# Performance work log

Measured on AMD Instinct MI355X. Metric: run time of the kernel, lower is better.

Reference implementation:

```python
import jax, jax.numpy as jnp
import numpy as np

D_MODEL = 512
N_HEADS = 8
D_HEAD = D_MODEL // N_HEADS  # 64
D_PROJ = 32
H_ENC = 512
D_MAX = 32


def _rope_cache(T, d):
    pos = jnp.arange(T, dtype=jnp.float32)[:, None]                      # [T,1]
    freqs = 1.0 / (10000.0 ** (jnp.arange(0, d, 2, dtype=jnp.float32) / d))  # [d/2]
    ang = pos * freqs                                                     # [T,d/2]
    return jnp.cos(ang), jnp.sin(ang)


def _apply_rope(x, cos, sin):
    # x: [B,H,T,D]
    T = x.shape[2]
    d2 = x.shape[-1] // 2
    x1, x2 = x[..., :d2], x[..., d2:]
    c = cos[:T][None, None]
    s = sin[:T][None, None]
    return jnp.concatenate([x1 * c - x2 * s, x2 * c + x1 * s], axis=-1)


def _layernorm(a, g, b, eps=1e-5):
    m = jnp.mean(a, axis=-1, keepdims=True)
    v = jnp.mean((a - m) ** 2, axis=-1, keepdims=True)
    return (a - m) * jax.lax.rsqrt(v + eps) * g + b


def setup_inputs() -> dict:
    key = jax.random.key(0)
    ks = jax.random.split(key, 8)
    B, T = 2, 2048
    x = jax.random.normal(ks[0], (B, T, D_MODEL), jnp.float32)
    q_projs = jax.random.normal(ks[1], (N_HEADS, D_MODEL, D_PROJ), jnp.float32) * D_MODEL ** -0.5
    k_projs = jax.random.normal(ks[2], (N_HEADS, D_MODEL, D_PROJ), jnp.float32) * D_MODEL ** -0.5
    w_v = jax.random.normal(ks[3], (D_MODEL, D_MODEL), jnp.float32) * D_MODEL ** -0.5
    w_proj = jax.random.normal(ks[4], (D_MODEL, D_MODEL), jnp.float32) * 0.02
    q_gain = jnp.ones((N_HEADS,), jnp.float32)
    enc_w0 = jax.random.normal(ks[5], (H_ENC, D_MODEL), jnp.float32) * D_MODEL ** -0.5
    enc_ln1_g = jnp.ones((H_ENC,), jnp.float32)
    enc_ln1_b = jnp.zeros((H_ENC,), jnp.float32)
    enc_w1 = jax.random.normal(ks[6], (H_ENC, H_ENC), jnp.float32) * H_ENC ** -0.5
    enc_ln2_g = jnp.ones((H_ENC,), jnp.float32)
    enc_ln2_b = jnp.zeros((H_ENC,), jnp.float32)
    enc_w2 = jax.random.normal(ks[7], (H_ENC, H_ENC), jnp.float32) * H_ENC ** -0.5
    enc_w_out = jax.random.normal(jax.random.fold_in(key, 99), (D_MAX, H_ENC), jnp.float32) * H_ENC ** -0.5
    coord_temp = jnp.ones((D_MAX,), jnp.float32)
    return {"x": x, "q_projs": q_projs, "k_projs": k_projs, "w_v": w_v, "w_proj": w_proj,
            "q_gain": q_gain, "enc_w0": enc_w0, "enc_ln1_g": enc_ln1_g, "enc_ln1_b": enc_ln1_b,
            "enc_w1": enc_w1, "enc_ln2_g": enc_ln2_g, "enc_ln2_b": enc_ln2_b, "enc_w2": enc_w2,
            "enc_w_out": enc_w_out, "coord_temp": coord_temp}


def reference(x, q_projs, k_projs, w_v, w_proj, q_gain,
              enc_w0, enc_ln1_g, enc_ln1_b, enc_w1, enc_ln2_g, enc_ln2_b,
              enc_w2, enc_w_out, coord_temp):
    B, T, C = x.shape
    # ---- CausalSelfAttention (qk_mode='per_head_proj') ----
    q = jnp.einsum('btd,hdo->bhto', x, q_projs)                    # [B,H,T,Dp]
    k = jnp.einsum('btd,hdo->bhto', x, k_projs)                    # [B,H,T,Dp]
    v = (x @ w_v.T).reshape(B, T, N_HEADS, D_HEAD).transpose(0, 2, 1, 3)  # [B,H,T,Dh]
    cos, sin = _rope_cache(T, D_PROJ)
    q = _apply_rope(q, cos, sin)
    k = _apply_rope(k, cos, sin)
    q = q * q_gain[None, :, None, None]
    scale = 1.0 / jnp.sqrt(jnp.asarray(D_PROJ, q.dtype))
    scores = jnp.einsum('bhto,bhso->bhts', q, k) * scale           # [B,H,T,T]
    causal = jnp.tril(jnp.ones((T, T), bool))
    scores = jnp.where(causal, scores, jnp.asarray(-1e30, scores.dtype))
    attn = jax.nn.softmax(scores, axis=-1)
    y = jnp.einsum('bhts,bhsd->bhtd', attn, v)                     # [B,H,T,Dh]
    # self-alignment subtraction (F.normalize eps = 1e-12)
    v_norm = v / jnp.maximum(jnp.linalg.norm(v, axis=-1, keepdims=True), 1e-12)
    self_align = jnp.sum(y * v_norm, axis=-1, keepdims=True) * v_norm
    y = y - self_align
    y = y.transpose(0, 2, 1, 3).reshape(B, T, C)
    h = x + y @ w_proj.T                                           # residual
    # ---- ChartEncoder (d_in == H so proj0 is Identity) ----
    he = h @ enc_w0.T
    he = h + jax.nn.silu(_layernorm(he, enc_ln1_g, enc_ln1_b) @ enc_w1.T)
    he = he + jax.nn.silu(_layernorm(he, enc_ln2_g, enc_ln2_b) @ enc_w2.T)
    h_rms = he * jax.lax.rsqrt(jnp.mean(he * he, axis=-1, keepdims=True) + 1e-6)
    z_raw = h_rms @ enc_w_out.T                                    # [B,T,d_max]
    z = jnp.tanh(z_raw / (jax.nn.softplus(coord_temp) + 1e-4))
    return z
```

## Files before the change

kernel.cpp:

```cpp
#include <hip/hip_runtime.h>
#include <math.h>

typedef unsigned short u16;
typedef __attribute__((ext_vector_type(8))) short short8;
typedef __attribute__((ext_vector_type(4))) float floatx4;

__device__ __forceinline__ float b2f(u16 u) { return __uint_as_float(((unsigned)u) << 16); }
__device__ __forceinline__ u16 f2b(float f) {
  unsigned u = __float_as_uint(f);
  return (u16)((u + 0x7fffu + ((u >> 16) & 1u)) >> 16);
}

__global__ __launch_bounds__(256) void prep_cast(const float* __restrict__ x, const float* __restrict__ wpr,
                                                 const float* __restrict__ w0, const float* __restrict__ w1,
                                                 const float* __restrict__ w2, const float* __restrict__ qp,
                                                 const float* __restrict__ kp, const float* __restrict__ wv,
                                                 u16* __restrict__ XB, u16* __restrict__ WPRb,
                                                 u16* __restrict__ W0b, u16* __restrict__ W1b,
                                                 u16* __restrict__ W2b, u16* __restrict__ wcat) {
  int bi = blockIdx.x, tid = threadIdx.x;
  if (bi < 2048) {
    int i = bi * 256 + tid;
    float4 v = ((const float4*)x)[i];
    ushort4 o; o.x = f2b(v.x); o.y = f2b(v.y); o.z = f2b(v.z); o.w = f2b(v.w);
    ((ushort4*)XB)[i] = o;
  } else if (bi < 3072) {
    int i = (bi - 2048) * 256 + tid;
    int sel = i >> 16, j = i & 65535;
    const float* s = sel == 0 ? wpr : sel == 1 ? w0 : sel == 2 ? w1 : w2;
    float4 v = ((const float4*)s)[j];
    ushort4 o; o.x = f2b(v.x); o.y = f2b(v.y); o.z = f2b(v.z); o.w = f2b(v.w);
    if (sel == 0) {
      ((ushort4*)WPRb)[j] = o;
    } else {
      u16* d = sel == 1 ? W0b : sel == 2 ? W1b : W2b;
      int n = j >> 7, k4 = (j & 127) << 2;
      int lane = (((k4 >> 3) & 3) << 4) | (n & 15);
      int dst = (((n >> 4) * 16 + (k4 >> 5)) << 9) + lane * 8 + (k4 & 7);
      *(ushort4*)(d + dst) = o;
    }
  } else {
    int i = (bi - 3072) * 256 + tid;
    int d = i & 511, c = i >> 9;
    float v;
    if (c < 512) {
      int hh = c >> 5, o = c & 31;
      const float* src = (hh < 8) ? qp : kp;
      int h = hh & 7;
      v = src[(h * 512 + d) * 32 + o];
    } else {
      v = wv[(c - 512) * 512 + d];
    }
    wcat[i] = f2b(v);
  }
}

template <int EPI, bool DUAL>
__global__ __launch_bounds__(256) void mgemm(const u16* __restrict__ A, const u16* __restrict__ Bw,
                                             const float* __restrict__ X, float* __restrict__ C,
                                             u16* __restrict__ Cb, int N) {
  __shared__ u16 As[64][72];
  __shared__ u16 Bs[64][72];
  const int tid = threadIdx.x;
  const int bm = blockIdx.y, bn = blockIdx.x;
  const int lane = tid & 63, wave = tid >> 6;
  const int wm = wave >> 1, wn = wave & 1;
  const int quad = lane >> 4, l16 = lane & 15;
  const int sr = tid >> 2;
  const int sk = (tid & 3) << 4;
  floatx4 acc[2][2] = {};
  const u16* Ap = A + (size_t)(bm * 64 + sr) * 512 + sk;
  const u16* Bp = Bw + (size_t)(bn * 64 + sr) * 512 + sk;
  uint4 a0 = *(const uint4*)(Ap);
  uint4 a1 = *(const uint4*)(Ap + 8);
  uint4 b0 = *(const uint4*)(Bp);
  uint4 b1 = *(const uint4*)(Bp + 8);
  for (int k0 = 0; k0 < 512; k0 += 64) {
    __syncthreads();
    *(uint4*)&As[sr][sk] = a0;
    *(uint4*)&As[sr][sk + 8] = a1;
    *(uint4*)&Bs[sr][sk] = b0;
    *(uint4*)&Bs[sr][sk + 8] = b1;
    __syncthreads();
    if (k0 + 64 < 512) {
      a0 = *(const uint4*)(Ap + k0 + 64);
      a1 = *(const uint4*)(Ap + k0 + 72);
      b0 = *(const uint4*)(Bp + k0 + 64);
      b1 = *(const uint4*)(Bp + k0 + 72);
    }
#pragma unroll
    for (int kk = 0; kk < 2; kk++) {
      short8 af0 = *(const short8*)&As[wm * 32 + l16][kk * 32 + quad * 8];
      short8 af1 = *(const short8*)&As[wm * 32 + 16 + l16][kk * 32 + quad * 8];
      short8 bf0 = *(const short8*)&Bs[wn * 32 + l16][kk * 32 + quad * 8];
      short8 bf1 = *(const short8*)&Bs[wn * 32 + 16 + l16][kk * 32 + quad * 8];
      acc[0][0] = __builtin_amdgcn_mfma_f32_16x16x32_bf16(af0, bf0, acc[0][0], 0, 0, 0);
      acc[0][1] = __builtin_amdgcn_mfma_f32_16x16x32_bf16(af0, bf1, acc[0][1], 0, 0, 0);
      acc[1][0] = __builtin_amdgcn_mfma_f32_16x16x32_bf16(af1, bf0, acc[1][0], 0, 0, 0);
      acc[1][1] = __builtin_amdgcn_mfma_f32_16x16x32_bf16(af1, bf1, acc[1][1], 0, 0, 0);
    }
  }
#pragma unroll
  for (int mt = 0; mt < 2; mt++)
#pragma unroll
    for (int r = 0; r < 4; r++) {
      int row = bm * 64 + wm * 32 + mt * 16 + quad * 4 + r;
#pragma unroll
      for (int nt = 0; nt < 2; nt++) {
        int col = bn * 64 + wn * 32 + nt * 16 + l16;
        float v = acc[mt][nt][r];
        if (EPI == 1) {
          v += X[(size_t)row * 512 + col];
        } else if (EPI == 2) {
          float xv = X[(size_t)row * 512 + col];
          v = xv + v / (1.f + __expf(-v));
        }
        C[(size_t)row * N + col] = v;
        if (DUAL) Cb[(size_t)row * N + col] = f2b(v);
      }
    }
}

__global__ __launch_bounds__(256) void prep_attn(const float* __restrict__ qkv, const float* __restrict__ qgain,
                                                 u16* __restrict__ qr, u16* __restrict__ kr,
                                                 u16* __restrict__ Vt) {
  const int bi = blockIdx.x, tid = threadIdx.x;
  if (bi < 2048) {
    int gid = bi * 256 + tid;
    int o = gid & 15;
    int t = (gid >> 4) & 2047;
    int h = (gid >> 15) & 7;
    int b = gid >> 18;
    const float* row = qkv + (size_t)(b * 2048 + t) * 1024;
    float freq = powf(10000.f, -(float)o / 16.f);
    float ang = (float)t * freq;
    float s, c;
    sincosf(ang, &s, &c);
    float g = qgain[h] * (0.17677669529663687f * 1.4426950408889634f);
    int qb = h * 32;
    float q0 = row[qb + o], q1 = row[qb + o + 16];
    float k0 = row[256 + qb + o], k1 = row[256 + qb + o + 16];
    u16* qo = qr + ((size_t)((b * 8 + h) * 2048 + t)) * 32;
    u16* ko = kr + ((size_t)((b * 8 + h) * 2048 + t)) * 32;
    qo[o] = f2b((q0 * c - q1 * s) * g);
    qo[o + 16] = f2b((q1 * c + q0 * s) * g);
    ko[o] = f2b(k0 * c - k1 * s);
    ko[o + 16] = f2b(k1 * c + k0 * s);
  } else {
    int idx = bi - 2048;
    const int tt = idx & 31, bh = idx >> 5;
    const int b = bh >> 3, h = bh & 7;
    __shared__ u16 Ts[64][72];
    const int r = tid >> 2, q = tid & 3;
    const float* src = qkv + ((size_t)(b * 2048 + tt * 64 + r)) * 1024 + 512 + h * 64 + q * 16;
#pragma unroll
    for (int j = 0; j < 4; j++) {
      float4 v = *(const float4*)(src + j * 4);
      Ts[q * 16 + j * 4 + 0][r] = f2b(v.x);
      Ts[q * 16 + j * 4 + 1][r] = f2b(v.y);
      Ts[q * 16 + j * 4 + 2][r] = f2b(v.z);
      Ts[q * 16 + j * 4 + 3][r] = f2b(v.w);
    }
    __syncthreads();
    u16* dst = Vt + ((size_t)(bh * 64 + r)) * 2048 + tt * 64 + q * 16;
    *(uint4*)dst = *(const uint4*)&Ts[r][q * 16];
    *(uint4*)(dst + 8) = *(const uint4*)&Ts[r][q * 16 + 8];
  }
}

__global__ __launch_bounds__(256) void attn_split(const u16* __restrict__ Qb, const u16* __restrict__ Kb,
                                                  const u16* __restrict__ Vt, float* __restrict__ PO,
                                                  float* __restrict__ PL) {
  const int bi = blockIdx.x;
  const int bh = bi & 15;
  const int q0i = (bi >> 4) & 15;
  const int rem = bi >> 8;
  const int qt = (rem & 1) ? (31 - q0i) : q0i;
  const int s = rem >> 1;
  const int tid = threadIdx.x;
  const int w = tid >> 6, lane = tid & 63, quad = lane >> 4, l16 = lane & 15;
  __shared__ u16 Vts[64][72];
  __shared__ u16 Ps[4][16][72];

  const int mid = (qt + 1) >> 1;
  const int kt_beg = s ? mid : 0;
  const int kt_end = s ? (qt + 1) : mid;

  short8 qfrag = *(const short8*)(Qb + ((size_t)(bh * 2048 + qt * 64 + w * 16 + l16)) * 32 + quad * 8);
  floatx4 o_acc[4] = {};
  float l_part[4] = {0.f, 0.f, 0.f, 0.f};
  const u16* Kbase = Kb + (size_t)bh * 2048 * 32;
  const u16* Vtb = Vt + (size_t)bh * 64 * 2048;
  const int vr = tid >> 2, vc = (tid & 3) << 4;

  uint4 v0 = {}, v1 = {};
  short8 kf[4] = {};
  if (kt_beg < kt_end) {
    const u16* src = Vtb + (size_t)vr * 2048 + kt_beg * 64 + vc;
    v0 = *(const uint4*)src;
    v1 = *(const uint4*)(src + 8);
#pragma unroll
    for (int nt = 0; nt < 4; nt++)
      kf[nt] = *(const short8*)(Kbase + (size_t)(kt_beg * 64 + nt * 16 + l16) * 32 + quad * 8);
  }

  for (int kt = kt_beg; kt < kt_end; ++kt) {
    __syncthreads();
    *(uint4*)&Vts[vr][vc] = v0;
    *(uint4*)&Vts[vr][vc + 8] = v1;
    __syncthreads();
    const bool more = (kt + 1 < kt_end);
    uint4 v0n = {}, v1n = {};
    short8 kfn[4] = {};
    if (more) {
      const u16* src = Vtb + (size_t)vr * 2048 + (kt + 1) * 64 + vc;
      v0n = *(const uint4*)src;
      v1n = *(const uint4*)(src + 8);
#pragma unroll
      for (int nt = 0; nt < 4; nt++)
        kfn[nt] = *(const short8*)(Kbase + (size_t)((kt + 1) * 64 + nt * 16 + l16) * 32 + quad * 8);
    }

    floatx4 s_acc[4];
#pragma unroll
    for (int nt = 0; nt < 4; nt++) {
      floatx4 zz = {0.f, 0.f, 0.f, 0.f};
      s_acc[nt] = __builtin_amdgcn_mfma_f32_16x16x32_bf16(qfrag, kf[nt], zz, 0, 0, 0);
    }
    const bool diag = (kt == qt);
#pragma unroll
    for (int r = 0; r < 4; r++) {
      int mloc = w * 16 + quad * 4 + r;
      float psum = 0.f;
#pragma unroll
      for (int nt = 0; nt < 4; nt++) {
        float p = __builtin_amdgcn_exp2f(s_acc[nt][r]);
        if (diag && (nt * 16 + l16) > mloc) p = 0.f;
        psum += p;
        Ps[w][quad * 4 + r][nt * 16 + l16] = f2b(p);
      }
      l_part[r] += psum;
    }
#pragma unroll
    for (int kc = 0; kc < 2; kc++) {
      short8 pf = *(const short8*)&Ps[w][l16][kc * 32 + quad * 8];
#pragma unroll
      for (int nt = 0; nt < 4; nt++) {
        short8 vf = *(const short8*)&Vts[nt * 16 + l16][kc * 32 + quad * 8];
        o_acc[nt] = __builtin_amdgcn_mfma_f32_16x16x32_bf16(pf, vf, o_acc[nt], 0, 0, 0);
      }
    }
    v0 = v0n; v1 = v1n;
#pragma unroll
    for (int nt = 0; nt < 4; nt++) kf[nt] = kfn[nt];
  }

  const int pidx = (bh * 32 + qt) * 2 + s;
  float* pob = PO + (size_t)pidx * 4096;
#pragma unroll
  for (int r = 0; r < 4; r++) {
    float ls = l_part[r];
#pragma unroll
    for (int mk = 1; mk < 16; mk <<= 1) ls += __shfl_xor(ls, mk, 64);
    int row = w * 16 + quad * 4 + r;
#pragma unroll
    for (int nt = 0; nt < 4; nt++) pob[row * 64 + nt * 16 + l16] = o_acc[nt][r];
    if (l16 == 0) PL[pidx * 64 + row] = ls;
  }
}

__global__ __launch_bounds__(256) void attn_combine(const float* __restrict__ PO, const float* __restrict__ PL,
                                                    const float* __restrict__ qkv, u16* __restrict__ y2b) {
  int ridx = blockIdx.x * 4 + (threadIdx.x >> 6);
  int lane = threadIdx.x & 63;
  int bh = ridx >> 11, tok = ridx & 2047;
  int qt = tok >> 6, row = tok & 63;
  int pidx = (bh * 32 + qt) * 2;
  const float* p0 = PO + (size_t)pidx * 4096 + row * 64;
  float o = p0[lane] + p0[4096 + lane];
  float l = PL[pidx * 64 + row] + PL[(pidx + 1) * 64 + row];
  float yv = o / l;
  int b = bh >> 3, h = bh & 7;
  float vv = qkv[(size_t)(b * 2048 + tok) * 1024 + 512 + h * 64 + lane];
  float ss = vv * vv, dot = yv * vv;
#pragma unroll
  for (int mk = 1; mk < 64; mk <<= 1) {
    ss += __shfl_xor(ss, mk, 64);
    dot += __shfl_xor(dot, mk, 64);
  }
  float coef = dot / fmaxf(ss, 1e-24f);
  y2b[(size_t)(b * 2048 + tok) * 512 + h * 64 + lane] = f2b(yv - coef * vv);
}

#define HPAD 516

__device__ __forceinline__ int enc_swz(int row, int col) {
  return row * 512 + ((((col >> 3) ^ (row & 7)) << 3) | (col & 7));
}

__device__ __forceinline__ void enc_gemm(const u16* __restrict__ inb, const u16* __restrict__ Wf,
                                         u16* __restrict__ Wst, floatx4* acc,
                                         int wave, int lane, int l16, int quad) {
  const int wslot = (wave * 4) * 512;
  const int src_lane = lane * 8;
#pragma unroll
  for (int nt = 0; nt < 4; nt++)
    __builtin_amdgcn_global_load_lds(
        (const __attribute__((address_space(1))) void*)(Wf + ((size_t)((wave * 4 + nt) * 16) << 9) + src_lane),
        (__attribute__((address_space(3))) void*)(Wst + wslot + nt * 512), 16, 0, 0);
  __syncthreads();
  for (int kc = 0; kc < 16; kc++) {
    const int cb = kc & 1;
    u16* bufC = Wst + cb * (8 * 4 * 512) + wslot;
    if (kc + 1 < 16) {
      u16* bufN = Wst + (cb ^ 1) * (8 * 4 * 512) + wslot;
#pragma unroll
      for (int nt = 0; nt < 4; nt++)
        __builtin_amdgcn_global_load_lds(
            (const __attribute__((address_space(1))) void*)(Wf + ((size_t)((wave * 4 + nt) * 16 + kc + 1) << 9) + src_lane),
            (__attribute__((address_space(3))) void*)(bufN + nt * 512), 16, 0, 0);
    }
    short8 af = *(const short8*)(inb + enc_swz(l16, kc * 32 + quad * 8));
#pragma unroll
    for (int nt = 0; nt < 4; nt++) {
      short8 bf = *(const short8*)(bufC + nt * 512 + src_lane);
      acc[nt] = __builtin_amdgcn_mfma_f32_16x16x32_bf16(af, bf, acc[nt], 0, 0, 0);
    }
    __syncthreads();
  }
}

__global__ __launch_bounds__(512) void enc_fused(const float* __restrict__ H, const u16* __restrict__ W0b,
                                                 const u16* __restrict__ W1b, const u16* __restrict__ W2b,
                                                 const float* __restrict__ g1v, const float* __restrict__ b1v,
                                                 const float* __restrict__ g2v, const float* __restrict__ b2v,
                                                 const float* __restrict__ wout, const float* __restrict__ ct,
                                                 float* __restrict__ z) {
  __shared__ u16 curb[16 * 512];
  __shared__ u16 lnb[16 * 512];
  __shared__ u16 Wst[2 * 8 * 4 * 512];
  __shared__ float hres[16][HPAD];
  __shared__ float red[8][16][2];

  const int tid = threadIdx.x;
  const int wave = tid >> 6, lane = tid & 63, quad = lane >> 4, l16 = lane & 15;
  const int row0 = blockIdx.x * 16;
  const int n0 = wave * 64;

#pragma unroll
  for (int j = 0; j < 4; j++) {
    int idx = j * 512 + tid;
    int row = idx >> 7, c4 = idx & 127;
    float4 v = ((const float4*)H)[(size_t)(row0 + row) * 128 + c4];
    *(float4*)&hres[row][c4 * 4] = v;
    int col = c4 * 4;
    curb[enc_swz(row, col + 0)] = f2b(v.x);
    curb[enc_swz(row, col + 1)] = f2b(v.y);
    curb[enc_swz(row, col + 2)] = f2b(v.z);
    curb[enc_swz(row, col + 3)] = f2b(v.w);
  }
  __syncthreads();

  floatx4 acc1[4] = {};
  enc_gemm(curb, W0b, Wst, acc1, wave, lane, l16, quad);

  {
#pragma unroll
    for (int r = 0; r < 4; r++) {
      float s = 0.f, q = 0.f;
#pragma unroll
      for (int nt = 0; nt < 4; nt++) { float v = acc1[nt][r]; s += v; q = fmaf(v, v, q); }
#pragma unroll
      for (int mk = 1; mk < 16; mk <<= 1) { s += __shfl_xor(s, mk, 64); q += __shfl_xor(q, mk, 64); }
      if (l16 == 0) { red[wave][quad * 4 + r][0] = s; red[wave][quad * 4 + r][1] = q; }
    }
    __syncthreads();
#pragma unroll
    for (int r = 0; r < 4; r++) {
      int R = quad * 4 + r;
      float st = 0.f, qt2 = 0.f;
#pragma unroll
      for (int w2 = 0; w2 < 8; w2++) { st += red[w2][R][0]; qt2 += red[w2][R][1]; }
      float mean = st * (1.f / 512.f);
      float inv = rsqrtf(qt2 * (1.f / 512.f) - mean * mean + 1e-5f);
#pragma unroll
      for (int nt = 0; nt < 4; nt++) {
        int col = n0 + nt * 16 + l16;
        lnb[enc_swz(R, col)] = f2b((acc1[nt][r] - mean) * inv * g1v[col] + b1v[col]);
      }
    }
    __syncthreads();
  }

  floatx4 acc2[4] = {};
  enc_gemm(lnb, W1b, Wst, acc2, wave, lane, l16, quad);
  float hval[4][4];
  {
#pragma unroll
    for (int r = 0; r < 4; r++) {
      int R = quad * 4 + r;
      float s = 0.f, q = 0.f;
#pragma unroll
      for (int nt = 0; nt < 4; nt++) {
        int col = n0 + nt * 16 + l16;
        float u = acc2[nt][r];
        float hv = hres[R][col] + u / (1.f + __expf(-u));
        hres[R][col] = hv;
        hval[nt][r] = hv;
        s += hv; q = fmaf(hv, hv, q);
      }
#pragma unroll
      for (int mk = 1; mk < 16; mk <<= 1) { s += __shfl_xor(s, mk, 64); q += __shfl_xor(q, mk, 64); }
      if (l16 == 0) { red[wave][R][0] = s; red[wave][R][1] = q; }
    }
    __syncthreads();
#pragma unroll
    for (int r = 0; r < 4; r++) {
      int R = quad * 4 + r;
      float st = 0.f, qt2 = 0.f;
#pragma unroll
      for (int w2 = 0; w2 < 8; w2++) { st += red[w2][R][0]; qt2 += red[w2][R][1]; }
      float mean = st * (1.f / 512.f);
      float inv = rsqrtf(qt2 * (1.f / 512.f) - mean * mean + 1e-5f);
#pragma unroll
      for (int nt = 0; nt < 4; nt++) {
        int col = n0 + nt * 16 + l16;
        lnb[enc_swz(R, col)] = f2b((hval[nt][r] - mean) * inv * g2v[col] + b2v[col]);
      }
    }
    __syncthreads();
  }

  floatx4 acc3[4] = {};
  enc_gemm(lnb, W2b, Wst, acc3, wave, lane, l16, quad);
  {
#pragma unroll
    for (int r = 0; r < 4; r++) {
      int R = quad * 4 + r;
      float q = 0.f;
#pragma unroll
      for (int nt = 0; nt < 4; nt++) {
        int col = n0 + nt * 16 + l16;
        float u = acc3[nt][r];
        float hv = hres[R][col] + u / (1.f + __expf(-u));
        hres[R][col] = hv;
        q = fmaf(hv, hv, q);
      }
#pragma unroll
      for (int mk = 1; mk < 16; mk <<= 1) q += __shfl_xor(q, mk, 64);
      if (l16 == 0) red[wave][R][1] = q;
    }
    __syncthreads();
  }

  {
    const int n = lane & 31, kh = lane >> 5;
    float rinv[2], pacc[2] = {0.f, 0.f};
#pragma unroll
    for (int rr = 0; rr < 2; rr++) {
      int R = wave * 2 + rr;
      float qt2 = 0.f;
#pragma unroll
      for (int w2 = 0; w2 < 8; w2++) qt2 += red[w2][R][1];
      rinv[rr] = rsqrtf(qt2 * (1.f / 512.f) + 1e-6f);
    }
    for (int kc = 0; kc < 64; kc++) {
      int k = kh * 256 + kc * 4;
      float4 wv = *(const float4*)(wout + (size_t)n * 512 + k);
#pragma unroll
      for (int rr = 0; rr < 2; rr++) {
        float4 hv = *(const float4*)&hres[wave * 2 + rr][k];
        pacc[rr] = fmaf(wv.x, hv.x, fmaf(wv.y, hv.y, fmaf(wv.z, hv.z, fmaf(wv.w, hv.w, pacc[rr]))));
      }
    }
#pragma unroll
    for (int rr = 0; rr < 2; rr++) pacc[rr] += __shfl_xor(pacc[rr], 32, 64);
    if (kh == 0) {
      float c = ct[n];
      float sp = (c > 20.f) ? c : log1pf(__expf(c));
#pragma unroll
      for (int rr = 0; rr < 2; rr++)
        z[(size_t)(row0 + wave * 2 + rr) * 32 + n] = tanhf(pacc[rr] * rinv[rr] / (sp + 1e-4f));
    }
  }
}

extern "C" void kernel_launch(void* const* d_in, const int* in_sizes, int n_in,
                              void* d_out, int out_size, void* d_ws, size_t ws_size,
                              hipStream_t stream) {
  const float* x = (const float*)d_in[0];
  const float* qp = (const float*)d_in[1];
  const float* kp = (const float*)d_in[2];
  const float* wv = (const float*)d_in[3];
  const float* wpr = (const float*)d_in[4];
  const float* qg = (const float*)d_in[5];
  const float* w0 = (const float*)d_in[6];
  const float* g1 = (const float*)d_in[7];
  const float* b1 = (const float*)d_in[8];
  const float* w1 = (const float*)d_in[9];
  const float* g2 = (const float*)d_in[10];
  const float* b2 = (const float*)d_in[11];
  const float* w2 = (const float*)d_in[12];
  const float* wout = (const float*)d_in[13];
  const float* ct = (const float*)d_in[14];
  float* z = (float*)d_out;

  float* ws = (float*)d_ws;
  const size_t MEG = 1024 * 1024;
  float* A_QKV = ws;
  u16* A_Qb = (u16*)(ws + 4 * MEG);
  u16* A_Kb = (u16*)(ws + 4 * MEG + 524288);
  u16* A_Vt = (u16*)(ws + 5 * MEG);
  float* A_PO = ws + 6 * MEG;
  u16* A_Y2b = (u16*)(ws + 10 * MEG);
  float* A_H = ws + 11 * MEG;
  u16* XB = (u16*)(ws + 13 * MEG);
  float* A_PL = ws + 13 * MEG;
  u16* WCATb = (u16*)(ws + 14 * MEG);
  u16* WPRb = WCATb + 524288;
  u16* W0b = WPRb + 262144;
  u16* W1b = W0b + 262144;
  u16* W2b = W1b + 262144;

  hipLaunchKernelGGL(prep_cast, dim3(5120), dim3(256), 0, stream, x, wpr, w0, w1, w2, qp, kp, wv,
                     XB, WPRb, W0b, W1b, W2b, WCATb);
  hipLaunchKernelGGL((mgemm<0, false>), dim3(16, 64), dim3(256), 0, stream, XB, WCATb,
                     (const float*)nullptr, A_QKV, (u16*)nullptr, 1024);
  hipLaunchKernelGGL(prep_attn, dim3(2560), dim3(256), 0, stream, A_QKV, qg, A_Qb, A_Kb, A_Vt);
  hipLaunchKernelGGL(attn_split, dim3(1024), dim3(256), 0, stream, A_Qb, A_Kb, A_Vt, A_PO, A_PL);
  hipLaunchKernelGGL(attn_combine, dim3(8192), dim3(256), 0, stream, A_PO, A_PL, A_QKV, A_Y2b);
  hipLaunchKernelGGL((mgemm<1, false>), dim3(8, 64), dim3(256), 0, stream, A_Y2b, WPRb, x, A_H,
                     (u16*)nullptr, 512);
  hipLaunchKernelGGL(enc_fused, dim3(256), dim3(512), 0, stream, A_H, W0b, W1b, W2b,
                     g1, b1, g2, b2, wout, ct, z);
}
```

Measured before the change: 202.1 us.

## Replace block barriers in encoder GEMM with per-wave vmcnt waits and stagger K order

Each wave stages only its own slice of the weight tile into LDS, so the encoder GEMM loop now drops the block-wide __syncthreads. Instead it waits on the wave's own async global-to-LDS loads with explicit s_waitcnt vmcnt, and the loop is fully unrolled with scheduling barriers. It also rotates the starting K chunk per group of blocks, so that concurrent blocks read different parts of the weight matrices. This targets barrier stalls and contention on the same weight rows, but relies on inline waitcnt and sched_barrier being correct for LDS visibility and can raise register and code-size pressure.

```diff
diff --git a/kernel.cpp b/kernel.cpp
--- a/kernel.cpp
+++ b/kernel.cpp
@@ -300,33 +300,40 @@
 
 __device__ __forceinline__ void enc_gemm(const u16* __restrict__ inb, const u16* __restrict__ Wf,
                                          u16* __restrict__ Wst, floatx4* acc,
-                                         int wave, int lane, int l16, int quad) {
-  const int wslot = (wave * 4) * 512;
-  const int src_lane = lane * 8;
+                                         int wave, int lane, int l16, int quad, int krot) {
+  const int wslot = wave * 4 * 512;
+  const int lo = lane * 8;
 #pragma unroll
   for (int nt = 0; nt < 4; nt++)
     __builtin_amdgcn_global_load_lds(
-        (const __attribute__((address_space(1))) void*)(Wf + ((size_t)((wave * 4 + nt) * 16) << 9) + src_lane),
+        (const __attribute__((address_space(1))) void*)(Wf + (((size_t)(wave * 4 + nt) * 16 + krot) << 9) + lo),
         (__attribute__((address_space(3))) void*)(Wst + wslot + nt * 512), 16, 0, 0);
-  __syncthreads();
-  for (int kc = 0; kc < 16; kc++) {
-    const int cb = kc & 1;
-    u16* bufC = Wst + cb * (8 * 4 * 512) + wslot;
-    if (kc + 1 < 16) {
-      u16* bufN = Wst + (cb ^ 1) * (8 * 4 * 512) + wslot;
+  __builtin_amdgcn_sched_barrier(0);
+#pragma unroll
+  for (int p = 0; p < 16; p++) {
+    if (p + 1 < 16) {
+      const int kn = (p + 1 + krot) & 15;
+      u16* bufN = Wst + ((p + 1) & 1) * (8 * 4 * 512) + wslot;
 #pragma unroll
       for (int nt = 0; nt < 4; nt++)
         __builtin_amdgcn_global_load_lds(
-            (const __attribute__((address_space(1))) void*)(Wf + ((size_t)((wave * 4 + nt) * 16 + kc + 1) << 9) + src_lane),
+            (const __attribute__((address_space(1))) void*)(Wf + (((size_t)(wave * 4 + nt) * 16 + kn) << 9) + lo),
             (__attribute__((address_space(3))) void*)(bufN + nt * 512), 16, 0, 0);
-    }
+      __builtin_amdgcn_sched_barrier(0);
+      asm volatile("s_waitcnt vmcnt(4)" ::: "memory");
+    } else {
+      asm volatile("s_waitcnt vmcnt(0)" ::: "memory");
+    }
+    __builtin_amdgcn_sched_barrier(0);
+    const u16* bufC = Wst + (p & 1) * (8 * 4 * 512) + wslot;
+    const int kc = (p + krot) & 15;
     short8 af = *(const short8*)(inb + enc_swz(l16, kc * 32 + quad * 8));
 #pragma unroll
     for (int nt = 0; nt < 4; nt++) {
-      short8 bf = *(const short8*)(bufC + nt * 512 + src_lane);
+      short8 bf = *(const short8*)(bufC + nt * 512 + lo);
       acc[nt] = __builtin_amdgcn_mfma_f32_16x16x32_bf16(af, bf, acc[nt], 0, 0, 0);
     }
-    __syncthreads();
+    __builtin_amdgcn_sched_barrier(0);
   }
 }
 
@@ -346,6 +353,7 @@
   const int wave = tid >> 6, lane = tid & 63, quad = lane >> 4, l16 = lane & 15;
   const int row0 = blockIdx.x * 16;
   const int n0 = wave * 64;
+  const int krot = (blockIdx.x >> 3) & 15;
 
 #pragma unroll
   for (int j = 0; j < 4; j++) {
@@ -362,7 +370,7 @@
   __syncthreads();
 
   floatx4 acc1[4] = {};
-  enc_gemm(curb, W0b, Wst, acc1, wave, lane, l16, quad);
+  enc_gemm(curb, W0b, Wst, acc1, wave, lane, l16, quad, krot);
 
   {
 #pragma unroll
@@ -393,7 +401,7 @@
   }
 
   floatx4 acc2[4] = {};
-  enc_gemm(lnb, W1b, Wst, acc2, wave, lane, l16, quad);
+  enc_gemm(lnb, W1b, Wst, acc2, wave, lane, l16, quad, krot);
   float hval[4][4];
   {
 #pragma unroll
@@ -432,7 +440,7 @@
   }
 
   floatx4 acc3[4] = {};
-  enc_gemm(lnb, W2b, Wst, acc3, wave, lane, l16, quad);
+  enc_gemm(lnb, W2b, Wst, acc3, wave, lane, l16, quad, krot);
   {
 #pragma unroll
     for (int r = 0; r < 4; r++) {
```

Result: faster. 188.3 us (-6.8%).
